# Optimization experiments

Hardware: AMD Instinct MI355X
Metric: run time of the kernel (lower is better)

The kernel has to match this reference:

```python
import jax, jax.numpy as jnp
import numpy as np

N, DIM, G, K = 100000, 512, 4, 16
GD = DIM // G
EPS = 1e-5

def _ln(x, g, b):
    mu = jnp.mean(x, axis=-1, keepdims=True)
    var = jnp.mean((x - mu) ** 2, axis=-1, keepdims=True)
    return (x - mu) / jnp.sqrt(var + EPS) * g + b

def setup_inputs() -> dict:
    key = jax.random.key(0)
    ks = jax.random.split(key, 12)
    s = 1.0 / np.sqrt(GD)
    return {
        "features": jax.random.normal(ks[0], (N, DIM), jnp.float32),
        "coords": jax.random.uniform(ks[1], (N, 3), jnp.float32),
        "neighbors": jax.random.randint(ks[2], (N, K), 0, N),
        "Wq": jax.random.normal(ks[3], (G, GD, GD), jnp.float32) * s,
        "Wk": jax.random.normal(ks[4], (G, GD, GD), jnp.float32) * s,
        "Wv": jax.random.normal(ks[5], (G, GD, GD), jnp.float32) * s,
        "Wo": jax.random.normal(ks[6], (DIM, DIM), jnp.float32) / np.sqrt(DIM),
        "bo": jnp.zeros((DIM,), jnp.float32),
        "ln1_g": jnp.ones((DIM,), jnp.float32),
        "ln1_b": jnp.zeros((DIM,), jnp.float32),
        "ln2_g": jnp.ones((DIM,), jnp.float32),
        "ln2_b": jnp.zeros((DIM,), jnp.float32),
        "W1": jax.random.normal(ks[7], (2 * DIM, DIM), jnp.float32) / np.sqrt(DIM),
        "b1": jnp.zeros((2 * DIM,), jnp.float32),
        "W2": jax.random.normal(ks[8], (DIM, 2 * DIM), jnp.float32) / np.sqrt(2 * DIM),
        "b2": jnp.zeros((DIM,), jnp.float32),
    }

def reference(features, coords, neighbors, Wq, Wk, Wv, Wo, bo, ln1_g, ln1_b, ln2_g, ln2_b, W1, b1, W2, b2):
    n = features.shape[0]
    residual = features
    x = _ln(features, ln1_g, ln1_b)
    xg = x.reshape(n, G, GD)                      # chunk along feature dim == group reshape
    # per-group Linear (no bias): y = x @ W.T with W (out,in)
    q = jnp.einsum('ngd,god->ngo', xg, Wq)
    k = jnp.einsum('ngd,god->ngo', xg, Wk)
    v = jnp.einsum('ngd,god->ngo', xg, Wv)
    nk = k[neighbors]                             # (N,K,G,GD) gather
    nv = v[neighbors]
    scale = jnp.asarray(1.0 / np.sqrt(GD), x.dtype)
    scores = jnp.einsum('ngd,nkgd->nkg', q, nk) * scale
    w = jax.nn.softmax(scores, axis=1)
    attn = jnp.einsum('nkg,nkgd->ngd', w, nv).reshape(n, DIM)
    out = attn @ Wo.T + bo + residual
    res2 = out
    y = _ln(out, ln2_g, ln2_b)
    y = jax.nn.gelu(y @ W1.T + b1, approximate=False) @ W2.T + b2
    return y + res2
```

## Files before the change

kernel.cpp:

```cpp
#include <hip/hip_runtime.h>
#include <hip/hip_bf16.h>
#include <math.h>

#define NPTS 100000
#define PAD_ROWS 100096
#define DIM 512
#define GRP 4
#define GD 128
#define K_NBR 16
#define EPS 1e-5f

using bf16x8 = __attribute__((ext_vector_type(8))) short;
using f32x4  = __attribute__((ext_vector_type(4))) float;
using short4v = __attribute__((ext_vector_type(4))) short;

__device__ inline float bf2f(short s) {
    unsigned u = ((unsigned)(unsigned short)s) << 16;
    union { unsigned u; float f; } c; c.u = u; return c.f;
}
__device__ inline short f2bf(float f) {
    union { float f; unsigned u; } c; c.f = f;
    unsigned u = c.u;
    unsigned r = (u + 0x7fffu + ((u >> 16) & 1u)) >> 16;
    return (short)r;
}

__device__ __forceinline__ void gload_lds16(short* lds, const short* g) {
    __builtin_amdgcn_global_load_lds(
        (const __attribute__((address_space(1))) unsigned int*)g,
        (__attribute__((address_space(3))) unsigned int*)lds, 16, 0, 0);
}

__global__ void cvt_kernel(const float* __restrict__ src, short* __restrict__ dst, int n) {
    int i = blockIdx.x * blockDim.x + threadIdx.x;
    int stride = gridDim.x * blockDim.x;
    for (; i < n; i += stride) dst[i] = f2bf(src[i]);
}

__global__ void prep_m_kernel(const float* __restrict__ wq, const float* __restrict__ wk,
                              short* __restrict__ mt) {
    int ge = blockIdx.x;
    int g = ge >> 7, e = ge & 127;
    int d = threadIdx.x;
    const float* Wq = wq + (size_t)g * GD * GD;
    const float* Wk = wk + (size_t)g * GD * GD;
    float acc = 0.0f;
    for (int o = 0; o < GD; ++o)
        acc += Wq[(size_t)o * GD + d] * Wk[(size_t)o * GD + e];
    mt[(size_t)ge * GD + d] = f2bf(acc * 0.08838834764831845f);
}

__global__ void prep_wov_kernel(const float* __restrict__ wo, const float* __restrict__ wv,
                                short* __restrict__ wov) {
    int o = blockIdx.x;
    int i = threadIdx.x;
    int g = i >> 7, i0 = i & 127;
    float acc = 0.0f;
    for (int d = 0; d < GD; ++d)
        acc += wo[(size_t)o * DIM + g * GD + d] * wv[((size_t)g * GD + d) * GD + i0];
    wov[(size_t)o * DIM + i] = f2bf(acc);
}

__global__ void ln_kernel(const float* __restrict__ in, const float* __restrict__ g,
                          const float* __restrict__ b, short* __restrict__ out) {
    int row = blockIdx.x;
    int tid = threadIdx.x;
    if (row >= NPTS) {
        short4v z; z[0] = 0; z[1] = 0; z[2] = 0; z[3] = 0;
        *(short4v*)(out + (size_t)row * DIM + tid * 4) = z;
        return;
    }
    const float4 x = *(const float4*)(in + (size_t)row * DIM + tid * 4);
    float s  = x.x + x.y + x.z + x.w;
    float sq = x.x * x.x + x.y * x.y + x.z * x.z + x.w * x.w;
    for (int m = 1; m < 64; m <<= 1) {
        s  += __shfl_xor(s, m);
        sq += __shfl_xor(sq, m);
    }
    __shared__ float ss[2], ssq[2];
    int wv = tid >> 6;
    if ((tid & 63) == 0) { ss[wv] = s; ssq[wv] = sq; }
    __syncthreads();
    s = ss[0] + ss[1]; sq = ssq[0] + ssq[1];
    float mu = s * (1.0f / DIM);
    float var = sq * (1.0f / DIM) - mu * mu;
    float rstd = rsqrtf(var + EPS);
    const float4 gg = *(const float4*)(g + tid * 4);
    const float4 bb = *(const float4*)(b + tid * 4);
    short4v o;
    o[0] = f2bf((x.x - mu) * rstd * gg.x + bb.x);
    o[1] = f2bf((x.y - mu) * rstd * gg.y + bb.y);
    o[2] = f2bf((x.z - mu) * rstd * gg.z + bb.z);
    o[3] = f2bf((x.w - mu) * rstd * gg.w + bb.w);
    *(short4v*)(out + (size_t)row * DIM + tid * 4) = o;
}

__global__ void ln_bf16_kernel(const short* __restrict__ in, const float* __restrict__ g,
                               const float* __restrict__ b, short* __restrict__ out) {
    int row = blockIdx.x;
    int tid = threadIdx.x;
    if (row >= NPTS) {
        short4v z; z[0] = 0; z[1] = 0; z[2] = 0; z[3] = 0;
        *(short4v*)(out + (size_t)row * DIM + tid * 4) = z;
        return;
    }
    short4v xi = *(const short4v*)(in + (size_t)row * DIM + tid * 4);
    float x0 = bf2f(xi[0]), x1 = bf2f(xi[1]), x2 = bf2f(xi[2]), x3 = bf2f(xi[3]);
    float s  = x0 + x1 + x2 + x3;
    float sq = x0 * x0 + x1 * x1 + x2 * x2 + x3 * x3;
    for (int m = 1; m < 64; m <<= 1) {
        s  += __shfl_xor(s, m);
        sq += __shfl_xor(sq, m);
    }
    __shared__ float ss[2], ssq[2];
    int wv = tid >> 6;
    if ((tid & 63) == 0) { ss[wv] = s; ssq[wv] = sq; }
    __syncthreads();
    s = ss[0] + ss[1]; sq = ssq[0] + ssq[1];
    float mu = s * (1.0f / DIM);
    float var = sq * (1.0f / DIM) - mu * mu;
    float rstd = rsqrtf(var + EPS);
    const float4 gg = *(const float4*)(g + tid * 4);
    const float4 bb = *(const float4*)(b + tid * 4);
    short4v o;
    o[0] = f2bf((x0 - mu) * rstd * gg.x + bb.x);
    o[1] = f2bf((x1 - mu) * rstd * gg.y + bb.y);
    o[2] = f2bf((x2 - mu) * rstd * gg.z + bb.z);
    o[3] = f2bf((x3 - mu) * rstd * gg.w + bb.w);
    *(short4v*)(out + (size_t)row * DIM + tid * 4) = o;
}

__device__ __forceinline__ void stage_tile(short* As, short* Bs,
        const short* aS, int as_, const short* bS, int bs_, int tid) {
    int ldRow = tid >> 2;
    int ldCol = (tid & 3) * 8;
    gload_lds16(As + (ldRow)      * 32 + ldCol, aS + (size_t)(ldRow)      * as_ + ldCol);
    gload_lds16(As + (ldRow + 64) * 32 + ldCol, aS + (size_t)(ldRow + 64) * as_ + ldCol);
    gload_lds16(Bs + (ldRow)      * 32 + ldCol, bS + (size_t)(ldRow)      * bs_ + ldCol);
    gload_lds16(Bs + (ldRow + 64) * 32 + ldCol, bS + (size_t)(ldRow + 64) * bs_ + ldCol);
}

__device__ __forceinline__ void compute_tile(const short* As, const short* Bs,
        int wr, int wc, int r, int ks, f32x4 (&acc)[4][4]) {
    bf16x8 a[4];
    #pragma unroll
    for (int m = 0; m < 4; ++m)
        a[m] = *(const bf16x8*)(As + (wr * 64 + m * 16 + r) * 32 + ks * 8);
    #pragma unroll
    for (int n = 0; n < 4; ++n) {
        bf16x8 b = *(const bf16x8*)(Bs + (wc * 64 + n * 16 + r) * 32 + ks * 8);
        #pragma unroll
        for (int m = 0; m < 4; ++m)
            acc[m][n] = __builtin_amdgcn_mfma_f32_16x16x32_bf16(a[m], b, acc[m][n], 0, 0, 0);
    }
}

template<int NK>
__device__ __forceinline__ void gemm_tile(
        const short* __restrict__ aBase, int as_,
        const short* __restrict__ bBase, int bs_,
        short* As0, short* Bs0, short* As1, short* Bs1, f32x4 (&acc)[4][4]) {
    int tid = threadIdx.x;
    int lane = tid & 63, wave = tid >> 6;
    int wr = wave >> 1, wc = wave & 1;
    int r = lane & 15, ks = lane >> 4;
    stage_tile(As0, Bs0, aBase, as_, bBase, bs_, tid);
    __syncthreads();
    #pragma unroll
    for (int kt = 0; kt < NK; kt += 2) {
        if (kt + 1 < NK)
            stage_tile(As1, Bs1, aBase + (kt + 1) * 32, as_, bBase + (kt + 1) * 32, bs_, tid);
        compute_tile(As0, Bs0, wr, wc, r, ks, acc);
        __syncthreads();
        if (kt + 2 < NK)
            stage_tile(As0, Bs0, aBase + (kt + 2) * 32, as_, bBase + (kt + 2) * 32, bs_, tid);
        compute_tile(As1, Bs1, wr, wc, r, ks, acc);
        __syncthreads();
    }
}

#define PB3 (128 * 32)
template<int NT>
__device__ __forceinline__ void gemmP3(
        const short* __restrict__ aBase, int as_,
        const short* __restrict__ bBase, int bs_,
        short* P, f32x4 (&acc)[4][4]) {
    int tid = threadIdx.x;
    int lane = tid & 63, wave = tid >> 6;
    int wr = wave >> 1, wc = wave & 1;
    int r = lane & 15, ks = lane >> 4;
    stage_tile(P,           P + PB3,           aBase,      as_, bBase,      bs_, tid);
    stage_tile(P + 2 * PB3, P + 3 * PB3,       aBase + 32, as_, bBase + 32, bs_, tid);
    #pragma unroll
    for (int t = 0; t < NT; ++t) {
        int bn = (t + 2) % 3, bc = t % 3;
        if (t + 2 < NT) {
            stage_tile(P + bn * 2 * PB3, P + bn * 2 * PB3 + PB3,
                       aBase + (size_t)(t + 2) * 32, as_,
                       bBase + (size_t)(t + 2) * 32, bs_, tid);
            asm volatile("s_waitcnt vmcnt(8)" ::: "memory");
        } else if (t + 1 < NT) {
            asm volatile("s_waitcnt vmcnt(4)" ::: "memory");
        } else {
            asm volatile("s_waitcnt vmcnt(0)" ::: "memory");
        }
        __builtin_amdgcn_s_barrier();
        __builtin_amdgcn_sched_barrier(0);
        compute_tile(P + bc * 2 * PB3, P + bc * 2 * PB3 + PB3, wr, wc, r, ks, acc);
        __builtin_amdgcn_s_barrier();
    }
}

#define GEMMP3_LDS __shared__ short P[6 * PB3]

__global__ __launch_bounds__(256) void qproj_kernel(
        const short* __restrict__ x, const short* __restrict__ mt,
        short* __restrict__ qp) {
    __shared__ short As0[128 * 32], Bs0[128 * 32], As1[128 * 32], Bs1[128 * 32];
    int nwg = gridDim.x;
    int bid = blockIdx.x;
    int tile = (bid & 7) * (nwg >> 3) + (bid >> 3);
    int rb = tile >> 2, g = tile & 3;
    int rowbase = rb * 128;
    int tid = threadIdx.x;
    int lane = tid & 63, wave = tid >> 6;
    int wr = wave >> 1, wc = wave & 1;
    int r = lane & 15, ks = lane >> 4;
    f32x4 acc[4][4];
    #pragma unroll
    for (int m = 0; m < 4; ++m)
        #pragma unroll
        for (int n = 0; n < 4; ++n)
            #pragma unroll
            for (int e = 0; e < 4; ++e) acc[m][n][e] = 0.0f;
    gemm_tile<4>(x + (size_t)rowbase * DIM + g * GD, DIM,
                 mt + (size_t)g * GD * GD, GD, As0, Bs0, As1, Bs1, acc);
    #pragma unroll
    for (int m = 0; m < 4; ++m)
        #pragma unroll
        for (int n = 0; n < 4; ++n)
            #pragma unroll
            for (int rr = 0; rr < 4; ++rr) {
                int orow = rowbase + wr * 64 + m * 16 + ks * 4 + rr;
                int lcol = wc * 64 + n * 16 + r;
                qp[(size_t)orow * DIM + g * GD + lcol] = f2bf(acc[m][n][rr]);
            }
}

__global__ __launch_bounds__(256) void attn_kernel(
        const short* __restrict__ qp, const short* __restrict__ x,
        const int* __restrict__ nbrs, short* __restrict__ t_out) {
    int b = blockIdx.x;
    int xcd = b & 7;
    int g = xcd >> 1;
    int quad = (b >> 3) * 2 + (xcd & 1);
    int tid = threadIdx.x;
    int wv = tid >> 6, lane = tid & 63;
    int n = quad * 4 + wv;
    int s = lane >> 4, t = lane & 15;
    int4 nbj = *(const int4*)(nbrs + (size_t)n * K_NBR + s * 4);
    int nbarr[4] = {nbj.x, nbj.y, nbj.z, nbj.w};
    size_t goff = (size_t)g * GD + t * 8;
    size_t qbase = (size_t)n * DIM + goff;
    bf16x8 qf = *(const bf16x8*)(qp + qbase);
    float qv[8];
    #pragma unroll
    for (int e = 0; e < 8; ++e) qv[e] = bf2f(qf[e]);
    bf16x8 xf[4];
    #pragma unroll
    for (int p = 0; p < 4; ++p)
        xf[p] = *(const bf16x8*)(x + (size_t)nbarr[p] * DIM + goff);
    float sc[4];
    #pragma unroll
    for (int p = 0; p < 4; ++p) {
        float dd = 0.0f;
        #pragma unroll
        for (int e = 0; e < 8; ++e) dd += qv[e] * bf2f(xf[p][e]);
        dd += __shfl_xor(dd, 1);
        dd += __shfl_xor(dd, 2);
        dd += __shfl_xor(dd, 4);
        dd += __shfl_xor(dd, 8);
        sc[p] = dd;
    }
    float mx = fmaxf(fmaxf(sc[0], sc[1]), fmaxf(sc[2], sc[3]));
    mx = fmaxf(mx, __shfl_xor(mx, 16));
    mx = fmaxf(mx, __shfl_xor(mx, 32));
    float ew[4]; float ssum = 0.0f;
    #pragma unroll
    for (int p = 0; p < 4; ++p) { ew[p] = __expf(sc[p] - mx); ssum += ew[p]; }
    ssum += __shfl_xor(ssum, 16);
    ssum += __shfl_xor(ssum, 32);
    float acc[8];
    #pragma unroll
    for (int d0 = 0; d0 < 8; ++d0) acc[d0] = 0.0f;
    #pragma unroll
    for (int p = 0; p < 4; ++p) {
        #pragma unroll
        for (int d0 = 0; d0 < 8; ++d0) acc[d0] += ew[p] * bf2f(xf[p][d0]);
    }
    #pragma unroll
    for (int d0 = 0; d0 < 8; ++d0) {
        acc[d0] += __shfl_xor(acc[d0], 16);
        acc[d0] += __shfl_xor(acc[d0], 32);
    }
    if (s == 0) {
        float inv = 1.0f / ssum;
        bf16x8 o;
        #pragma unroll
        for (int d0 = 0; d0 < 8; ++d0) o[d0] = f2bf(acc[d0] * inv);
        *(bf16x8*)(t_out + qbase) = o;
    }
}

__global__ __launch_bounds__(256) void outproj_kernel(
        const short* __restrict__ tbuf, const short* __restrict__ wov,
        const float* __restrict__ bo, const float* __restrict__ features,
        short* __restrict__ res2) {
    GEMMP3_LDS;
    int nwg = gridDim.x;
    int bid = blockIdx.x;
    int tile = (bid & 7) * (nwg >> 3) + (bid >> 3);
    int rb = tile >> 2, cb = tile & 3;
    int rowbase = rb * 128, colbase = cb * 128;
    int tid = threadIdx.x;
    int lane = tid & 63, wave = tid >> 6;
    int wr = wave >> 1, wc = wave & 1;
    int r = lane & 15, ks = lane >> 4;
    f32x4 acc[4][4];
    #pragma unroll
    for (int m = 0; m < 4; ++m)
        #pragma unroll
        for (int n = 0; n < 4; ++n)
            #pragma unroll
            for (int e = 0; e < 4; ++e) acc[m][n][e] = 0.0f;
    gemmP3<16>(tbuf + (size_t)rowbase * DIM, DIM,
               wov + (size_t)colbase * DIM, DIM, P, acc);
    #pragma unroll
    for (int m = 0; m < 4; ++m)
        #pragma unroll
        for (int n = 0; n < 4; ++n)
            #pragma unroll
            for (int rr = 0; rr < 4; ++rr) {
                int orow = rowbase + wr * 64 + m * 16 + ks * 4 + rr;
                int ocol = colbase + wc * 64 + n * 16 + r;
                if (orow < NPTS) {
                    float val = acc[m][n][rr] + bo[ocol] + features[(size_t)orow * DIM + ocol];
                    res2[(size_t)orow * DIM + ocol] = f2bf(val);
                }
            }
}

__global__ __launch_bounds__(256) void ffn1_kernel(
        const short* __restrict__ y, const short* __restrict__ w1,
        const float* __restrict__ b1, short* __restrict__ h) {
    GEMMP3_LDS;
    int nwg = gridDim.x;
    int bid = blockIdx.x;
    int tile = (bid & 7) * (nwg >> 3) + (bid >> 3);
    int rb = tile >> 3, cb = tile & 7;
    int rowbase = rb * 128, colbase = cb * 128;
    int tid = threadIdx.x;
    int lane = tid & 63, wave = tid >> 6;
    int wr = wave >> 1, wc = wave & 1;
    int r = lane & 15, ks = lane >> 4;
    f32x4 acc[4][4];
    #pragma unroll
    for (int m = 0; m < 4; ++m)
        #pragma unroll
        for (int n = 0; n < 4; ++n)
            #pragma unroll
            for (int e = 0; e < 4; ++e) acc[m][n][e] = 0.0f;
    gemmP3<16>(y + (size_t)rowbase * DIM, DIM,
               w1 + (size_t)colbase * DIM, DIM, P, acc);
    #pragma unroll
    for (int m = 0; m < 4; ++m)
        #pragma unroll
        for (int n = 0; n < 4; ++n)
            #pragma unroll
            for (int rr = 0; rr < 4; ++rr) {
                int orow = rowbase + wr * 64 + m * 16 + ks * 4 + rr;
                int ocol = colbase + wc * 64 + n * 16 + r;
                float xv = acc[m][n][rr] + b1[ocol];
                float xc = fminf(fmaxf(xv, -9.0f), 9.0f);
                float u = xc * (0.7978845608028654f + 0.0356774081f * xc * xc);
                float e2 = __expf(2.0f * u);
                float th = (e2 - 1.0f) / (e2 + 1.0f);
                float gl = 0.5f * xv * (1.0f + th);
                h[(size_t)orow * (2 * DIM) + ocol] = f2bf(gl);
            }
}

__global__ __launch_bounds__(256) void ffn2_kernel(
        const short* __restrict__ h, const short* __restrict__ w2,
        const float* __restrict__ b2, const short* __restrict__ res2,
        float* __restrict__ out) {
    GEMMP3_LDS;
    int nwg = gridDim.x;
    int bid = blockIdx.x;
    int tile = (bid & 7) * (nwg >> 3) + (bid >> 3);
    int rb = tile >> 2, cb = tile & 3;
    int rowbase = rb * 128, colbase = cb * 128;
    int tid = threadIdx.x;
    int lane = tid & 63, wave = tid >> 6;
    int wr = wave >> 1, wc = wave & 1;
    int r = lane & 15, ks = lane >> 4;
    f32x4 acc[4][4];
    #pragma unroll
    for (int m = 0; m < 4; ++m)
        #pragma unroll
        for (int n = 0; n < 4; ++n)
            #pragma unroll
            for (int e = 0; e < 4; ++e) acc[m][n][e] = 0.0f;
    gemmP3<32>(h + (size_t)rowbase * (2 * DIM), 2 * DIM,
               w2 + (size_t)colbase * (2 * DIM), 2 * DIM, P, acc);
    #pragma unroll
    for (int m = 0; m < 4; ++m)
        #pragma unroll
        for (int n = 0; n < 4; ++n)
            #pragma unroll
            for (int rr = 0; rr < 4; ++rr) {
                int orow = rowbase + wr * 64 + m * 16 + ks * 4 + rr;
                int ocol = colbase + wc * 64 + n * 16 + r;
                if (orow < NPTS) {
                    size_t idx = (size_t)orow * DIM + ocol;
                    out[idx] = acc[m][n][rr] + b2[ocol] + bf2f(res2[idx]);
                }
            }
}

extern "C" void kernel_launch(void* const* d_in, const int* in_sizes, int n_in,
                              void* d_out, int out_size, void* d_ws, size_t ws_size,
                              hipStream_t stream) {
    const float* features = (const float*)d_in[0];
    const int*   neighbors = (const int*)d_in[2];
    const float* Wq = (const float*)d_in[3];
    const float* Wk = (const float*)d_in[4];
    const float* Wv = (const float*)d_in[5];
    const float* Wo = (const float*)d_in[6];
    const float* bo = (const float*)d_in[7];
    const float* ln1_g = (const float*)d_in[8];
    const float* ln1_b = (const float*)d_in[9];
    const float* ln2_g = (const float*)d_in[10];
    const float* ln2_b = (const float*)d_in[11];
    const float* W1 = (const float*)d_in[12];
    const float* b1 = (const float*)d_in[13];
    const float* W2 = (const float*)d_in[14];
    const float* b2 = (const float*)d_in[15];
    float* out = (float*)d_out;

    size_t slotElems = (size_t)PAD_ROWS * DIM;
    short* s0 = (short*)d_ws;
    short* s1 = s0 + slotElems;
    short* s2 = s1 + slotElems;
    short* s3 = s2 + slotElems;
    short* mt_b  = s3 + slotElems;
    short* wov_b = mt_b + GRP * GD * GD;
    short* w1_b  = wov_b + DIM * DIM;
    short* w2_b  = w1_b + 2 * DIM * DIM;

    cvt_kernel<<<256, 256, 0, stream>>>(W1, w1_b, 2 * DIM * DIM);
    cvt_kernel<<<256, 256, 0, stream>>>(W2, w2_b, 2 * DIM * DIM);
    prep_m_kernel<<<GRP * GD, GD, 0, stream>>>(Wq, Wk, mt_b);
    prep_wov_kernel<<<DIM, DIM, 0, stream>>>(Wo, Wv, wov_b);

    ln_kernel<<<PAD_ROWS, 128, 0, stream>>>(features, ln1_g, ln1_b, s0);

    qproj_kernel<<<(PAD_ROWS / 128) * 4, 256, 0, stream>>>(s0, mt_b, s1);

    attn_kernel<<<NPTS, 256, 0, stream>>>(s1, s0, neighbors, s2);

    outproj_kernel<<<(PAD_ROWS / 128) * 4, 256, 0, stream>>>(s2, wov_b, bo, features, s3);

    ln_bf16_kernel<<<PAD_ROWS, 128, 0, stream>>>(s3, ln2_g, ln2_b, s0);

    ffn1_kernel<<<(PAD_ROWS / 128) * 8, 256, 0, stream>>>(s0, w1_b, b1, s1);

    ffn2_kernel<<<(PAD_ROWS / 128) * 4, 256, 0, stream>>>(s1, w2_b, b2, s3, out);
}
```

Before: 1.075 ms.

## Load GEMM B operand directly into registers, stage only A through LDS

Replaces the triple-buffered GEMM helper with a variant that stages only the activation (A) tile through LDS. Each wave now loads its weight (B) fragments straight from global memory into registers, double-buffered one k-step ahead. This halves the LDS footprint and LDS traffic and is meant to raise occupancy. The cost is redundant B loads across waves sharing a column (wr=0/1) and more VGPR pressure. The hand-tuned vmcnt waits must still match the count of outstanding loads.

```diff
diff --git a/kernel.cpp b/kernel.cpp
--- a/kernel.cpp
+++ b/kernel.cpp
@@ -179,9 +179,17 @@
     }
 }
 
-#define PB3 (128 * 32)
+#define APB (128 * 32)
+
+__device__ __forceinline__ void stageA(short* As, const short* aS, int as_, int tid) {
+    int ldRow = tid >> 2;
+    int ldCol = (tid & 3) * 8;
+    gload_lds16(As + (ldRow)      * 32 + ldCol, aS + (size_t)(ldRow)      * as_ + ldCol);
+    gload_lds16(As + (ldRow + 64) * 32 + ldCol, aS + (size_t)(ldRow + 64) * as_ + ldCol);
+}
+
 template<int NT>
-__device__ __forceinline__ void gemmP3(
+__device__ __forceinline__ void gemmH(
         const short* __restrict__ aBase, int as_,
         const short* __restrict__ bBase, int bs_,
         short* P, f32x4 (&acc)[4][4]) {
@@ -189,29 +197,43 @@
     int lane = tid & 63, wave = tid >> 6;
     int wr = wave >> 1, wc = wave & 1;
     int r = lane & 15, ks = lane >> 4;
-    stage_tile(P,           P + PB3,           aBase,      as_, bBase,      bs_, tid);
-    stage_tile(P + 2 * PB3, P + 3 * PB3,       aBase + 32, as_, bBase + 32, bs_, tid);
-    #pragma unroll
+    const short* bp = bBase + (size_t)(wc * 64 + r) * bs_ + ks * 8;
+    stageA(P,       aBase,      as_, tid);
+    stageA(P + APB, aBase + 32, as_, tid);
+    bf16x8 bcur[4], bnext[4];
+    #pragma unroll
+    for (int n = 0; n < 4; ++n)
+        bcur[n] = *(const bf16x8*)(bp + (size_t)n * 16 * bs_);
     for (int t = 0; t < NT; ++t) {
-        int bn = (t + 2) % 3, bc = t % 3;
-        if (t + 2 < NT) {
-            stage_tile(P + bn * 2 * PB3, P + bn * 2 * PB3 + PB3,
-                       aBase + (size_t)(t + 2) * 32, as_,
-                       bBase + (size_t)(t + 2) * 32, bs_, tid);
+        if (t + 2 < NT)
+            stageA(P + ((t + 2) % 3) * APB, aBase + (size_t)(t + 2) * 32, as_, tid);
+        if (t + 1 < NT) {
+            #pragma unroll
+            for (int n = 0; n < 4; ++n)
+                bnext[n] = *(const bf16x8*)(bp + (size_t)n * 16 * bs_ + (t + 1) * 32);
+            asm volatile("s_waitcnt vmcnt(12)" ::: "memory");
+        } else {
             asm volatile("s_waitcnt vmcnt(8)" ::: "memory");
-        } else if (t + 1 < NT) {
-            asm volatile("s_waitcnt vmcnt(4)" ::: "memory");
-        } else {
-            asm volatile("s_waitcnt vmcnt(0)" ::: "memory");
         }
         __builtin_amdgcn_s_barrier();
         __builtin_amdgcn_sched_barrier(0);
-        compute_tile(P + bc * 2 * PB3, P + bc * 2 * PB3 + PB3, wr, wc, r, ks, acc);
+        const short* As = P + (t % 3) * APB;
+        bf16x8 a[4];
+        #pragma unroll
+        for (int m = 0; m < 4; ++m)
+            a[m] = *(const bf16x8*)(As + (wr * 64 + m * 16 + r) * 32 + ks * 8);
+        #pragma unroll
+        for (int n = 0; n < 4; ++n)
+            #pragma unroll
+            for (int m = 0; m < 4; ++m)
+                acc[m][n] = __builtin_amdgcn_mfma_f32_16x16x32_bf16(a[m], bcur[n], acc[m][n], 0, 0, 0);
         __builtin_amdgcn_s_barrier();
-    }
-}
-
-#define GEMMP3_LDS __shared__ short P[6 * PB3]
+        #pragma unroll
+        for (int n = 0; n < 4; ++n) bcur[n] = bnext[n];
+    }
+}
+
+#define GEMMH_LDS __shared__ short P[3 * APB]
 
 __global__ __launch_bounds__(256) void qproj_kernel(
         const short* __restrict__ x, const short* __restrict__ mt,
@@ -316,7 +338,7 @@
         const short* __restrict__ tbuf, const short* __restrict__ wov,
         const float* __restrict__ bo, const float* __restrict__ features,
         short* __restrict__ res2) {
-    GEMMP3_LDS;
+    GEMMH_LDS;
     int nwg = gridDim.x;
     int bid = blockIdx.x;
     int tile = (bid & 7) * (nwg >> 3) + (bid >> 3);
@@ -333,8 +355,8 @@
         for (int n = 0; n < 4; ++n)
             #pragma unroll
             for (int e = 0; e < 4; ++e) acc[m][n][e] = 0.0f;
-    gemmP3<16>(tbuf + (size_t)rowbase * DIM, DIM,
-               wov + (size_t)colbase * DIM, DIM, P, acc);
+    gemmH<16>(tbuf + (size_t)rowbase * DIM, DIM,
+              wov + (size_t)colbase * DIM, DIM, P, acc);
     #pragma unroll
     for (int m = 0; m < 4; ++m)
         #pragma unroll
@@ -353,7 +375,7 @@
 __global__ __launch_bounds__(256) void ffn1_kernel(
         const short* __restrict__ y, const short* __restrict__ w1,
         const float* __restrict__ b1, short* __restrict__ h) {
-    GEMMP3_LDS;
+    GEMMH_LDS;
     int nwg = gridDim.x;
     int bid = blockIdx.x;
     int tile = (bid & 7) * (nwg >> 3) + (bid >> 3);
@@ -370,8 +392,8 @@
         for (int n = 0; n < 4; ++n)
             #pragma unroll
             for (int e = 0; e < 4; ++e) acc[m][n][e] = 0.0f;
-    gemmP3<16>(y + (size_t)rowbase * DIM, DIM,
-               w1 + (size_t)colbase * DIM, DIM, P, acc);
+    gemmH<16>(y + (size_t)rowbase * DIM, DIM,
+              w1 + (size_t)colbase * DIM, DIM, P, acc);
     #pragma unroll
     for (int m = 0; m < 4; ++m)
         #pragma unroll
@@ -394,7 +416,7 @@
         const short* __restrict__ h, const short* __restrict__ w2,
         const float* __restrict__ b2, const short* __restrict__ res2,
         float* __restrict__ out) {
-    GEMMP3_LDS;
+    GEMMH_LDS;
     int nwg = gridDim.x;
     int bid = blockIdx.x;
     int tile = (bid & 7) * (nwg >> 3) + (bid >> 3);
@@ -411,8 +433,8 @@
         for (int n = 0; n < 4; ++n)
             #pragma unroll
             for (int e = 0; e < 4; ++e) acc[m][n][e] = 0.0f;
-    gemmP3<32>(h + (size_t)rowbase * (2 * DIM), 2 * DIM,
-               w2 + (size_t)colbase * (2 * DIM), 2 * DIM, P, acc);
+    gemmH<32>(h + (size_t)rowbase * (2 * DIM), 2 * DIM,
+              w2 + (size_t)colbase * (2 * DIM), 2 * DIM, P, acc);
     #pragma unroll
     for (int m = 0; m < 4; ++m)
         #pragma unroll
```

New measurement: 1.240 ms. 1.15x slower.
